# Optimization experiments

Measured on AMD Instinct MI355X. Metric: run time of the kernel, lower is better.

## Reference

```python
import jax, jax.numpy as jnp
import numpy as np

N = 50000          # nodes
E = 800000         # edges (avg degree 16)
IN_C = 3
HEADS = 4
NUM_GRAPHS = 8
NUM_CLASSES = 10


def setup_inputs() -> dict:
    key = jax.random.key(0)
    ks = jax.random.split(key, 12)
    x = jax.random.normal(ks[0], (N, IN_C), jnp.float32)
    edge_index = jax.random.randint(ks[1], (2, E), 0, N, dtype=jnp.int64)
    batch = jnp.sort(jax.random.randint(ks[2], (N,), 0, NUM_GRAPHS, dtype=jnp.int64))

    def glorot(k, shape, fan):
        return jax.random.normal(k, shape, jnp.float32) * np.float32(1.0 / np.sqrt(fan))

    return {
        "x": x, "edge_index": edge_index, "batch": batch,
        "fc0_w": glorot(ks[3], (IN_C, 16), IN_C), "fc0_b": jnp.zeros((16,), jnp.float32),
        "u1": glorot(ks[4], (16, HEADS), 16), "c1": jnp.zeros((HEADS,), jnp.float32),
        "w1": glorot(ks[5], (16, HEADS * 32), 16), "b1": jnp.zeros((32,), jnp.float32),
        "u2": glorot(ks[6], (32, HEADS), 32), "c2": jnp.zeros((HEADS,), jnp.float32),
        "w2": glorot(ks[7], (32, HEADS * 64), 32), "b2": jnp.zeros((64,), jnp.float32),
        "fc1_w": glorot(ks[8], (64, NUM_CLASSES), 64), "fc1_b": jnp.zeros((NUM_CLASSES,), jnp.float32),
    }


def feast_conv(x, src, dst, u, c, w, b, heads, out_c):
    """FeaStConv (t_inv=True): per-edge head softmax on (x_j - x_i), mean aggregation."""
    n = x.shape[0]
    # soft-assignment over heads: [E, H]
    q = jax.nn.softmax((x[src] - x[dst]) @ u + c, axis=-1)
    # transform at node level, then gather per edge: [E, H, out_c]
    xw = (x @ w).reshape(n, heads, out_c)
    msg = jnp.einsum('eh,ehc->ec', q, xw[src])           # [E, out_c]
    agg = jax.ops.segment_sum(msg, dst, num_segments=n)  # sum over incoming edges
    cnt = jax.ops.segment_sum(jnp.ones((src.shape[0],), x.dtype), dst, num_segments=n)
    return agg / jnp.maximum(cnt, 1.0)[:, None] + b


def global_mean_pool(x, batch, num_graphs):
    s = jax.ops.segment_sum(x, batch, num_segments=num_graphs)
    cnt = jax.ops.segment_sum(jnp.ones((x.shape[0],), x.dtype), batch, num_segments=num_graphs)
    return s / jnp.maximum(cnt, 1.0)[:, None]


def reference(x, edge_index, batch, fc0_w, fc0_b, u1, c1, w1, b1, u2, c2, w2, b2, fc1_w, fc1_b):
    src, dst = edge_index[0], edge_index[1]   # x_j = x[src], x_i = x[dst]
    h = jax.nn.relu(x @ fc0_w + fc0_b)                              # [N, 16]
    h = jax.nn.relu(feast_conv(h, src, dst, u1, c1, w1, b1, HEADS, 32))  # [N, 32]
    h = jax.nn.relu(feast_conv(h, src, dst, u2, c2, w2, b2, HEADS, 64))  # [N, 64]
    g = global_mean_pool(h, batch, NUM_GRAPHS)                      # [G, 64]
    # dropout is identity in eval mode
    return g @ fc1_w + fc1_b                                        # [G, num_classes]
```

## Files before the change

kernel.cpp:

```cpp
#include <hip/hip_runtime.h>

#define N_NODES 50000
#define N_EDGES 800000
#define HEADS 4
#define NUM_GRAPHS 8

#define EBLK ((N_EDGES + 255) / 256)
#define NBLK ((N_NODES + 255) / 256)

__global__ __launch_bounds__(256) void hist_fc0_kernel(
    const int* __restrict__ dst, int* __restrict__ deg, int* __restrict__ off,
    const float* __restrict__ x,
    const float* __restrict__ fc0_w, const float* __restrict__ fc0_b,
    const float* __restrict__ u1,
    float* __restrict__ h0, float* __restrict__ P1) {
  if (blockIdx.x < EBLK) {
    int e = blockIdx.x * 256 + threadIdx.x;
    if (e < N_EDGES) off[e] = atomicAdd(&deg[dst[e]], 1);
    return;
  }
  __shared__ float sW0[3 * 16];
  __shared__ float sB0[16];
  __shared__ float sU[16 * 4];
  for (int i = threadIdx.x; i < 48; i += 256) sW0[i] = fc0_w[i];
  for (int i = threadIdx.x; i < 16; i += 256) sB0[i] = fc0_b[i];
  for (int i = threadIdx.x; i < 64; i += 256) sU[i] = u1[i];
  __syncthreads();
  int n = (blockIdx.x - EBLK) * 256 + threadIdx.x;
  if (n >= N_NODES) return;
  float x0 = x[n * 3 + 0], x1 = x[n * 3 + 1], x2 = x[n * 3 + 2];
  float h[16];
#pragma unroll
  for (int j = 0; j < 16; j++) {
    float v = x0 * sW0[0 * 16 + j] + x1 * sW0[1 * 16 + j] + x2 * sW0[2 * 16 + j] + sB0[j];
    h[j] = fmaxf(v, 0.f);
    h0[(size_t)n * 16 + j] = h[j];
  }
  float p0 = 0.f, p1 = 0.f, p2 = 0.f, p3 = 0.f;
#pragma unroll
  for (int j = 0; j < 16; j++) {
    p0 += h[j] * sU[j * 4 + 0];
    p1 += h[j] * sU[j * 4 + 1];
    p2 += h[j] * sU[j * 4 + 2];
    p3 += h[j] * sU[j * 4 + 3];
  }
  reinterpret_cast<float4*>(P1)[n] = make_float4(p0, p1, p2, p3);
}

__global__ __launch_bounds__(256) void alloc_kernel(const int* __restrict__ deg,
                                                    int* __restrict__ gctr,
                                                    int* __restrict__ rowstart) {
  int i = blockIdx.x * blockDim.x + threadIdx.x;
  int lane = threadIdx.x & 63;
  int d = (i < N_NODES) ? deg[i] : 0;
  int pre = d;
#pragma unroll
  for (int offd = 1; offd < 64; offd <<= 1) {
    int v = __shfl_up(pre, offd, 64);
    if (lane >= offd) pre += v;
  }
  int total = __shfl(pre, 63, 64);
  int base = 0;
  if (lane == 63) base = atomicAdd(gctr, total);
  base = __shfl(base, 63, 64);
  if (i < N_NODES) rowstart[i] = base + pre - d;
}

__global__ __launch_bounds__(256) void scatter_kernel(const int* __restrict__ src,
                                                      const int* __restrict__ dst,
                                                      const int* __restrict__ rowstart,
                                                      const int* __restrict__ off,
                                                      int* __restrict__ src_perm) {
  int e = blockIdx.x * blockDim.x + threadIdx.x;
  if (e >= N_EDGES) return;
  src_perm[rowstart[dst[e]] + off[e]] = src[e];
}

__device__ __forceinline__ float4 edge_q(float4 Ps, float b0, float b1, float b2, float b3) {
  float l0 = Ps.x + b0, l1 = Ps.y + b1, l2 = Ps.z + b2, l3 = Ps.w + b3;
  float m = fmaxf(fmaxf(l0, l1), fmaxf(l2, l3));
  float e0 = __expf(l0 - m), e1 = __expf(l1 - m), e2 = __expf(l2 - m), e3 = __expf(l3 - m);
  float inv = 1.f / (e0 + e1 + e2 + e3);
  return make_float4(e0 * inv, e1 * inv, e2 * inv, e3 * inv);
}

__global__ __launch_bounds__(256) void agg1_kernel(
    const int* __restrict__ rowstart, const int* __restrict__ deg,
    const int* __restrict__ src_perm,
    const float* __restrict__ P1, const float* __restrict__ c1,
    const float* __restrict__ h0,
    float* __restrict__ A) {
  int wave = threadIdx.x >> 6;
  int lane = threadIdx.x & 63;
  int g = lane >> 4;
  int j = lane & 15;
  int node = blockIdx.x * 4 + wave;
  if (node >= N_NODES) return;
  float4 Pd = reinterpret_cast<const float4*>(P1)[node];
  float b0 = c1[0] - Pd.x, b1 = c1[1] - Pd.y, b2 = c1[2] - Pd.z, b3 = c1[3] - Pd.w;
  int e0 = rowstart[node];
  int e1 = e0 + deg[node];
  const float4* P4 = reinterpret_cast<const float4*>(P1);
  float a0 = 0.f, a1 = 0.f, a2 = 0.f, a3 = 0.f;
  int p = e0;
  for (; p + 16 <= e1; p += 16) {
    int sA = src_perm[p + 0 + g];
    int sB = src_perm[p + 4 + g];
    int sC = src_perm[p + 8 + g];
    int sD = src_perm[p + 12 + g];
    float4 PA = P4[sA];
    float4 PB = P4[sB];
    float4 PC = P4[sC];
    float4 PD = P4[sD];
    float fA = h0[(size_t)sA * 16 + j];
    float fB = h0[(size_t)sB * 16 + j];
    float fC = h0[(size_t)sC * 16 + j];
    float fD = h0[(size_t)sD * 16 + j];
    float4 qA = edge_q(PA, b0, b1, b2, b3);
    float4 qB = edge_q(PB, b0, b1, b2, b3);
    float4 qC = edge_q(PC, b0, b1, b2, b3);
    float4 qD = edge_q(PD, b0, b1, b2, b3);
    a0 += qA.x * fA + qB.x * fB + qC.x * fC + qD.x * fD;
    a1 += qA.y * fA + qB.y * fB + qC.y * fC + qD.y * fD;
    a2 += qA.z * fA + qB.z * fB + qC.z * fC + qD.z * fD;
    a3 += qA.w * fA + qB.w * fB + qC.w * fC + qD.w * fD;
  }
  for (; p + 4 <= e1; p += 4) {
    int s = src_perm[p + g];
    float4 Ps = P4[s];
    float f = h0[(size_t)s * 16 + j];
    float4 q = edge_q(Ps, b0, b1, b2, b3);
    a0 += q.x * f; a1 += q.y * f; a2 += q.z * f; a3 += q.w * f;
  }
  int rem = e1 - p;
  if (g < rem) {
    int s = src_perm[p + g];
    float4 Ps = P4[s];
    float f = h0[(size_t)s * 16 + j];
    float4 q = edge_q(Ps, b0, b1, b2, b3);
    a0 += q.x * f; a1 += q.y * f; a2 += q.z * f; a3 += q.w * f;
  }
  a0 += __shfl_xor(a0, 16, 64); a0 += __shfl_xor(a0, 32, 64);
  a1 += __shfl_xor(a1, 16, 64); a1 += __shfl_xor(a1, 32, 64);
  a2 += __shfl_xor(a2, 16, 64); a2 += __shfl_xor(a2, 32, 64);
  a3 += __shfl_xor(a3, 16, 64); a3 += __shfl_xor(a3, 32, 64);
  float o = (g == 0) ? a0 : (g == 1) ? a1 : (g == 2) ? a2 : a3;
  A[(size_t)node * 64 + lane] = o;
}

__global__ __launch_bounds__(256) void agg2_kernel(
    const int* __restrict__ rowstart, const int* __restrict__ deg,
    const int* __restrict__ src_perm,
    const float* __restrict__ P2, const float* __restrict__ c2,
    const float* __restrict__ h1,
    float* __restrict__ A) {
  int wave = threadIdx.x >> 6;
  int lane = threadIdx.x & 63;
  int g = lane >> 5;
  int j = lane & 31;
  int node = blockIdx.x * 4 + wave;
  if (node >= N_NODES) return;
  float4 Pd = reinterpret_cast<const float4*>(P2)[node];
  float b0 = c2[0] - Pd.x, b1 = c2[1] - Pd.y, b2 = c2[2] - Pd.z, b3 = c2[3] - Pd.w;
  int e0 = rowstart[node];
  int e1 = e0 + deg[node];
  const float4* P4 = reinterpret_cast<const float4*>(P2);
  float a0 = 0.f, a1 = 0.f, a2 = 0.f, a3 = 0.f;
  int p = e0;
  for (; p + 8 <= e1; p += 8) {
    int sA = src_perm[p + 0 + g];
    int sB = src_perm[p + 2 + g];
    int sC = src_perm[p + 4 + g];
    int sD = src_perm[p + 6 + g];
    float4 PA = P4[sA];
    float4 PB = P4[sB];
    float4 PC = P4[sC];
    float4 PD = P4[sD];
    float fA = h1[(size_t)sA * 32 + j];
    float fB = h1[(size_t)sB * 32 + j];
    float fC = h1[(size_t)sC * 32 + j];
    float fD = h1[(size_t)sD * 32 + j];
    float4 qA = edge_q(PA, b0, b1, b2, b3);
    float4 qB = edge_q(PB, b0, b1, b2, b3);
    float4 qC = edge_q(PC, b0, b1, b2, b3);
    float4 qD = edge_q(PD, b0, b1, b2, b3);
    a0 += qA.x * fA + qB.x * fB + qC.x * fC + qD.x * fD;
    a1 += qA.y * fA + qB.y * fB + qC.y * fC + qD.y * fD;
    a2 += qA.z * fA + qB.z * fB + qC.z * fC + qD.z * fD;
    a3 += qA.w * fA + qB.w * fB + qC.w * fC + qD.w * fD;
  }
  for (; p + 2 <= e1; p += 2) {
    int s = src_perm[p + g];
    float4 Ps = P4[s];
    float f = h1[(size_t)s * 32 + j];
    float4 q = edge_q(Ps, b0, b1, b2, b3);
    a0 += q.x * f; a1 += q.y * f; a2 += q.z * f; a3 += q.w * f;
  }
  int rem = e1 - p;
  if (g < rem) {
    int s = src_perm[p + g];
    float4 Ps = P4[s];
    float f = h1[(size_t)s * 32 + j];
    float4 q = edge_q(Ps, b0, b1, b2, b3);
    a0 += q.x * f; a1 += q.y * f; a2 += q.z * f; a3 += q.w * f;
  }
  a0 += __shfl_xor(a0, 32, 64);
  a1 += __shfl_xor(a1, 32, 64);
  a2 += __shfl_xor(a2, 32, 64);
  a3 += __shfl_xor(a3, 32, 64);
  float oa = (g == 0) ? a0 : a1;
  float ob = (g == 0) ? a2 : a3;
  A[(size_t)node * 128 + lane] = oa;
  A[(size_t)node * 128 + 64 + lane] = ob;
}

__global__ __launch_bounds__(256) void gemm1_kernel(
    const int* __restrict__ deg, const float* __restrict__ A,
    const float* __restrict__ w1, const float* __restrict__ b1,
    const float* __restrict__ u2,
    float* __restrict__ h1, float* __restrict__ P2) {
  __shared__ float sB[64 * 32];
  __shared__ float sU[32 * 4];
  for (int i = threadIdx.x; i < 64 * 32; i += 256) {
    int hj = i / 32, c = i % 32;
    sB[i] = w1[(hj % 16) * 128 + (hj / 16) * 32 + c];
  }
  for (int i = threadIdx.x; i < 128; i += 256) sU[i] = u2[i];
  __syncthreads();
  const float4* sB4 = reinterpret_cast<const float4*>(sB);
  int c4 = threadIdx.x & 7;
  int g = threadIdx.x >> 3;
  int n0 = blockIdx.x * 64 + g * 2;
  int n1 = n0 + 1;
  int na = min(n0, N_NODES - 1);
  int nb = min(n1, N_NODES - 1);
  const float4* A0 = reinterpret_cast<const float4*>(A + (size_t)na * 64);
  const float4* A1 = reinterpret_cast<const float4*>(A + (size_t)nb * 64);
  float4 bc = reinterpret_cast<const float4*>(b1)[c4];
  float4 acc0 = {0, 0, 0, 0}, acc1 = {0, 0, 0, 0};
#pragma unroll 2
  for (int k4 = 0; k4 < 16; k4++) {
    float4 a0 = A0[k4];
    float4 a1 = A1[k4];
    float4 w0 = sB4[(4 * k4 + 0) * 8 + c4];
    float4 wv1 = sB4[(4 * k4 + 1) * 8 + c4];
    float4 w2v = sB4[(4 * k4 + 2) * 8 + c4];
    float4 w3 = sB4[(4 * k4 + 3) * 8 + c4];
    acc0.x += a0.x * w0.x + a0.y * wv1.x + a0.z * w2v.x + a0.w * w3.x;
    acc0.y += a0.x * w0.y + a0.y * wv1.y + a0.z * w2v.y + a0.w * w3.y;
    acc0.z += a0.x * w0.z + a0.y * wv1.z + a0.z * w2v.z + a0.w * w3.z;
    acc0.w += a0.x * w0.w + a0.y * wv1.w + a0.z * w2v.w + a0.w * w3.w;
    acc1.x += a1.x * w0.x + a1.y * wv1.x + a1.z * w2v.x + a1.w * w3.x;
    acc1.y += a1.x * w0.y + a1.y * wv1.y + a1.z * w2v.y + a1.w * w3.y;
    acc1.z += a1.x * w0.z + a1.y * wv1.z + a1.z * w2v.z + a1.w * w3.z;
    acc1.w += a1.x * w0.w + a1.y * wv1.w + a1.z * w2v.w + a1.w * w3.w;
  }
  float inv0 = 1.f / fmaxf((float)deg[na], 1.f);
  float inv1 = 1.f / fmaxf((float)deg[nb], 1.f);
  float4 o0 = {fmaxf(acc0.x * inv0 + bc.x, 0.f), fmaxf(acc0.y * inv0 + bc.y, 0.f),
               fmaxf(acc0.z * inv0 + bc.z, 0.f), fmaxf(acc0.w * inv0 + bc.w, 0.f)};
  float4 o1 = {fmaxf(acc1.x * inv1 + bc.x, 0.f), fmaxf(acc1.y * inv1 + bc.y, 0.f),
               fmaxf(acc1.z * inv1 + bc.z, 0.f), fmaxf(acc1.w * inv1 + bc.w, 0.f)};
  if (n0 < N_NODES) reinterpret_cast<float4*>(h1 + (size_t)n0 * 32)[c4] = o0;
  if (n1 < N_NODES) reinterpret_cast<float4*>(h1 + (size_t)n1 * 32)[c4] = o1;
  float pa[4] = {0, 0, 0, 0}, pb[4] = {0, 0, 0, 0};
#pragma unroll
  for (int k = 0; k < 4; k++) {
    int c = 4 * c4 + k;
    float v0 = k == 0 ? o0.x : k == 1 ? o0.y : k == 2 ? o0.z : o0.w;
    float v1 = k == 0 ? o1.x : k == 1 ? o1.y : k == 2 ? o1.z : o1.w;
#pragma unroll
    for (int hh = 0; hh < 4; hh++) {
      pa[hh] += v0 * sU[c * 4 + hh];
      pb[hh] += v1 * sU[c * 4 + hh];
    }
  }
#pragma unroll
  for (int msk = 1; msk <= 4; msk <<= 1) {
#pragma unroll
    for (int hh = 0; hh < 4; hh++) {
      pa[hh] += __shfl_xor(pa[hh], msk, 64);
      pb[hh] += __shfl_xor(pb[hh], msk, 64);
    }
  }
  if (c4 == 0) {
    if (n0 < N_NODES)
      reinterpret_cast<float4*>(P2)[n0] = make_float4(pa[0], pa[1], pa[2], pa[3]);
    if (n1 < N_NODES)
      reinterpret_cast<float4*>(P2)[n1] = make_float4(pb[0], pb[1], pb[2], pb[3]);
  }
}

__global__ __launch_bounds__(256) void gemm2_kernel(
    const int* __restrict__ deg, const float* __restrict__ A,
    const float* __restrict__ w2, const float* __restrict__ b2,
    float* __restrict__ h2) {
  __shared__ float sB[128 * 64];
  for (int i = threadIdx.x; i < 128 * 64; i += 256) {
    int hj = i / 64, c = i % 64;
    sB[i] = w2[(hj % 32) * 256 + (hj / 32) * 64 + c];
  }
  __syncthreads();
  const float4* sB4 = reinterpret_cast<const float4*>(sB);
  int c4 = threadIdx.x & 15;
  int g = threadIdx.x >> 4;
  int n0 = blockIdx.x * 32 + g * 2;
  int n1 = n0 + 1;
  int na = min(n0, N_NODES - 1);
  int nb = min(n1, N_NODES - 1);
  const float4* A0 = reinterpret_cast<const float4*>(A + (size_t)na * 128);
  const float4* A1 = reinterpret_cast<const float4*>(A + (size_t)nb * 128);
  float4 bc = reinterpret_cast<const float4*>(b2)[c4];
  float4 acc0 = {0, 0, 0, 0}, acc1 = {0, 0, 0, 0};
#pragma unroll 2
  for (int k4 = 0; k4 < 32; k4++) {
    float4 a0 = A0[k4];
    float4 a1 = A1[k4];
    float4 w0 = sB4[(4 * k4 + 0) * 16 + c4];
    float4 wv1 = sB4[(4 * k4 + 1) * 16 + c4];
    float4 w2v = sB4[(4 * k4 + 2) * 16 + c4];
    float4 w3 = sB4[(4 * k4 + 3) * 16 + c4];
    acc0.x += a0.x * w0.x + a0.y * wv1.x + a0.z * w2v.x + a0.w * w3.x;
    acc0.y += a0.x * w0.y + a0.y * wv1.y + a0.z * w2v.y + a0.w * w3.y;
    acc0.z += a0.x * w0.z + a0.y * wv1.z + a0.z * w2v.z + a0.w * w3.z;
    acc0.w += a0.x * w0.w + a0.y * wv1.w + a0.z * w2v.w + a0.w * w3.w;
    acc1.x += a1.x * w0.x + a1.y * wv1.x + a1.z * w2v.x + a1.w * w3.x;
    acc1.y += a1.x * w0.y + a1.y * wv1.y + a1.z * w2v.y + a1.w * w3.y;
    acc1.z += a1.x * w0.z + a1.y * wv1.z + a1.z * w2v.z + a1.w * w3.z;
    acc1.w += a1.x * w0.w + a1.y * wv1.w + a1.z * w2v.w + a1.w * w3.w;
  }
  if (n0 < N_NODES) {
    float inv = 1.f / fmaxf((float)deg[n0], 1.f);
    float4 o = {fmaxf(acc0.x * inv + bc.x, 0.f), fmaxf(acc0.y * inv + bc.y, 0.f),
                fmaxf(acc0.z * inv + bc.z, 0.f), fmaxf(acc0.w * inv + bc.w, 0.f)};
    reinterpret_cast<float4*>(h2 + (size_t)n0 * 64)[c4] = o;
  }
  if (n1 < N_NODES) {
    float inv = 1.f / fmaxf((float)deg[n1], 1.f);
    float4 o = {fmaxf(acc1.x * inv + bc.x, 0.f), fmaxf(acc1.y * inv + bc.y, 0.f),
                fmaxf(acc1.z * inv + bc.z, 0.f), fmaxf(acc1.w * inv + bc.w, 0.f)};
    reinterpret_cast<float4*>(h2 + (size_t)n1 * 64)[c4] = o;
  }
}

#define POOL_CHUNK 64
__global__ __launch_bounds__(256) void pool_kernel(
    const float* __restrict__ h2, const int* __restrict__ batch,
    float* __restrict__ gsum, float* __restrict__ gcnt) {
  int grp = threadIdx.x / 64;
  int c = threadIdx.x % 64;
  int n0 = (blockIdx.x * 4 + grp) * POOL_CHUNK;
  int n1 = min(n0 + POOL_CHUNK, N_NODES);
  if (n0 >= N_NODES) return;
  float acc = 0.f;
  float cacc = 0.f;
  int curg = batch[n0];
  for (int n = n0; n < n1; n++) {
    int g = batch[n];
    float v = h2[(size_t)n * 64 + c];
    if (g != curg) {
      atomicAdd(&gsum[curg * 64 + c], acc);
      if (c == 0) atomicAdd(&gcnt[curg], cacc);
      acc = 0.f;
      cacc = 0.f;
      curg = g;
    }
    acc += v;
    cacc += 1.f;
  }
  atomicAdd(&gsum[curg * 64 + c], acc);
  if (c == 0) atomicAdd(&gcnt[curg], cacc);
}

__global__ __launch_bounds__(128) void head_kernel(
    const float* __restrict__ gsum, const float* __restrict__ gcnt,
    const float* __restrict__ fc1_w, const float* __restrict__ fc1_b,
    float* __restrict__ out) {
  int t = threadIdx.x;
  if (t >= NUM_GRAPHS * 10) return;
  int g = t / 10, k = t % 10;
  float inv = 1.f / fmaxf(gcnt[g], 1.f);
  float s = fc1_b[k];
#pragma unroll
  for (int c = 0; c < 64; c++) s += gsum[g * 64 + c] * inv * fc1_w[c * 10 + k];
  out[g * 10 + k] = s;
}

extern "C" void kernel_launch(void* const* d_in, const int* in_sizes, int n_in,
                              void* d_out, int out_size, void* d_ws, size_t ws_size,
                              hipStream_t stream) {
  const float* x = (const float*)d_in[0];
  const int* edge_index = (const int*)d_in[1];
  const int* batch = (const int*)d_in[2];
  const float* fc0_w = (const float*)d_in[3];
  const float* fc0_b = (const float*)d_in[4];
  const float* u1 = (const float*)d_in[5];
  const float* c1 = (const float*)d_in[6];
  const float* w1 = (const float*)d_in[7];
  const float* b1 = (const float*)d_in[8];
  const float* u2 = (const float*)d_in[9];
  const float* c2 = (const float*)d_in[10];
  const float* w2 = (const float*)d_in[11];
  const float* b2 = (const float*)d_in[12];
  const float* fc1_w = (const float*)d_in[13];
  const float* fc1_b = (const float*)d_in[14];
  float* out = (float*)d_out;

  const int* src = edge_index;
  const int* dst = edge_index + N_EDGES;

  char* wsb = (char*)d_ws;
  int* deg = (int*)wsb;
  int* gctr = deg + N_NODES;
  float* gsum = (float*)wsb + 50004;
  float* gcnt = gsum + NUM_GRAPHS * 64;
  int* rowstart = (int*)wsb + 50524;
  int* off = rowstart + N_NODES;
  int* src_perm = off + N_EDGES;
  float* h0 = (float*)wsb + 1700524;
  float* h1 = h0 + (size_t)N_NODES * 16;
  float* h2 = h1 + (size_t)N_NODES * 32;
  float* A = h2 + (size_t)N_NODES * 64;
  float* P1 = A + (size_t)N_NODES * 128;
  float* P2 = P1 + (size_t)N_NODES * 4;

  hipMemsetAsync(d_ws, 0, 50524 * sizeof(int), stream);

  int nblk = NBLK;
  int eblk = EBLK;
  int wblk = (N_NODES + 3) / 4;

  hist_fc0_kernel<<<eblk + nblk, 256, 0, stream>>>(dst, deg, off, x, fc0_w, fc0_b, u1, h0, P1);
  alloc_kernel<<<nblk, 256, 0, stream>>>(deg, gctr, rowstart);
  scatter_kernel<<<eblk, 256, 0, stream>>>(src, dst, rowstart, off, src_perm);

  agg1_kernel<<<wblk, 256, 0, stream>>>(rowstart, deg, src_perm, P1, c1, h0, A);
  gemm1_kernel<<<(N_NODES + 63) / 64, 256, 0, stream>>>(deg, A, w1, b1, u2, h1, P2);

  agg2_kernel<<<wblk, 256, 0, stream>>>(rowstart, deg, src_perm, P2, c2, h1, A);
  gemm2_kernel<<<(N_NODES + 31) / 32, 256, 0, stream>>>(deg, A, w2, b2, h2);

  int pblk = (N_NODES + POOL_CHUNK * 4 - 1) / (POOL_CHUNK * 4);
  pool_kernel<<<pblk, 256, 0, stream>>>(h2, batch, gsum, gcnt);
  head_kernel<<<1, 128, 0, stream>>>(gsum, gcnt, fc1_w, fc1_b, out);
}
```

Baseline: 273.3 us.

## Fuse gemm2 with global mean pooling and classifier head via last-block pattern

The layer-2 GEMM epilogue now accumulates each node's output directly into per-block shared-memory graph sums, then flushes them with global atomics. This removes the h2 write and reread and the separate pool kernel. The last block to finish, detected with an atomic counter, computes the final classifier output, which removes the head kernel launch. In exchange it adds shared and global atomics plus a threadfence and counter handshake, and relies on batch being sorted so that most blocks span at most two graphs.

```diff
diff --git a/kernel.cpp b/kernel.cpp
--- a/kernel.cpp
+++ b/kernel.cpp
@@ -291,20 +291,35 @@
   }
 }
 
-__global__ __launch_bounds__(256) void gemm2_kernel(
+__global__ __launch_bounds__(256) void gemm2_pool_kernel(
     const int* __restrict__ deg, const float* __restrict__ A,
     const float* __restrict__ w2, const float* __restrict__ b2,
-    float* __restrict__ h2) {
+    const int* __restrict__ batch,
+    float* __restrict__ gsum, float* __restrict__ gcnt, int* __restrict__ done,
+    const float* __restrict__ fc1_w, const float* __restrict__ fc1_b,
+    float* __restrict__ out) {
   __shared__ float sB[128 * 64];
+  __shared__ float sg[2][64];
+  __shared__ float scnt[2];
+  __shared__ int sgmin, sgmax, islast;
   for (int i = threadIdx.x; i < 128 * 64; i += 256) {
     int hj = i / 64, c = i % 64;
     sB[i] = w2[(hj % 32) * 256 + (hj / 32) * 64 + c];
   }
+  if (threadIdx.x < 128) sg[threadIdx.x >> 6][threadIdx.x & 63] = 0.f;
+  if (threadIdx.x < 2) scnt[threadIdx.x] = 0.f;
+  if (threadIdx.x == 0) {
+    int base = (int)blockIdx.x * 32;
+    int last = base + 31;
+    if (last > N_NODES - 1) last = N_NODES - 1;
+    sgmin = batch[base];
+    sgmax = batch[last];
+  }
   __syncthreads();
   const float4* sB4 = reinterpret_cast<const float4*>(sB);
   int c4 = threadIdx.x & 15;
   int g = threadIdx.x >> 4;
-  int n0 = blockIdx.x * 32 + g * 2;
+  int n0 = (int)blockIdx.x * 32 + g * 2;
   int n1 = n0 + 1;
   int na = min(n0, N_NODES - 1);
   int nb = min(n1, N_NODES - 1);
@@ -329,61 +344,76 @@
     acc1.z += a1.x * w0.z + a1.y * wv1.z + a1.z * w2v.z + a1.w * w3.z;
     acc1.w += a1.x * w0.w + a1.y * wv1.w + a1.z * w2v.w + a1.w * w3.w;
   }
+  float inv0 = 1.f / fmaxf((float)deg[na], 1.f);
+  float inv1 = 1.f / fmaxf((float)deg[nb], 1.f);
+  float4 o0 = {fmaxf(acc0.x * inv0 + bc.x, 0.f), fmaxf(acc0.y * inv0 + bc.y, 0.f),
+               fmaxf(acc0.z * inv0 + bc.z, 0.f), fmaxf(acc0.w * inv0 + bc.w, 0.f)};
+  float4 o1 = {fmaxf(acc1.x * inv1 + bc.x, 0.f), fmaxf(acc1.y * inv1 + bc.y, 0.f),
+               fmaxf(acc1.z * inv1 + bc.z, 0.f), fmaxf(acc1.w * inv1 + bc.w, 0.f)};
+  int gmin = sgmin;
   if (n0 < N_NODES) {
-    float inv = 1.f / fmaxf((float)deg[n0], 1.f);
-    float4 o = {fmaxf(acc0.x * inv + bc.x, 0.f), fmaxf(acc0.y * inv + bc.y, 0.f),
-                fmaxf(acc0.z * inv + bc.z, 0.f), fmaxf(acc0.w * inv + bc.w, 0.f)};
-    reinterpret_cast<float4*>(h2 + (size_t)n0 * 64)[c4] = o;
+    int b0v = batch[na];
+    int slot = b0v - gmin;
+    if (slot <= 1) {
+      atomicAdd(&sg[slot][c4 * 4 + 0], o0.x);
+      atomicAdd(&sg[slot][c4 * 4 + 1], o0.y);
+      atomicAdd(&sg[slot][c4 * 4 + 2], o0.z);
+      atomicAdd(&sg[slot][c4 * 4 + 3], o0.w);
+      if (c4 == 0) atomicAdd(&scnt[slot], 1.f);
+    } else {
+      atomicAdd(&gsum[b0v * 64 + c4 * 4 + 0], o0.x);
+      atomicAdd(&gsum[b0v * 64 + c4 * 4 + 1], o0.y);
+      atomicAdd(&gsum[b0v * 64 + c4 * 4 + 2], o0.z);
+      atomicAdd(&gsum[b0v * 64 + c4 * 4 + 3], o0.w);
+      if (c4 == 0) atomicAdd(&gcnt[b0v], 1.f);
+    }
   }
   if (n1 < N_NODES) {
-    float inv = 1.f / fmaxf((float)deg[n1], 1.f);
-    float4 o = {fmaxf(acc1.x * inv + bc.x, 0.f), fmaxf(acc1.y * inv + bc.y, 0.f),
-                fmaxf(acc1.z * inv + bc.z, 0.f), fmaxf(acc1.w * inv + bc.w, 0.f)};
-    reinterpret_cast<float4*>(h2 + (size_t)n1 * 64)[c4] = o;
-  }
-}
-
-#define POOL_CHUNK 64
-__global__ __launch_bounds__(256) void pool_kernel(
-    const float* __restrict__ h2, const int* __restrict__ batch,
-    float* __restrict__ gsum, float* __restrict__ gcnt) {
-  int grp = threadIdx.x / 64;
-  int c = threadIdx.x % 64;
-  int n0 = (blockIdx.x * 4 + grp) * POOL_CHUNK;
-  int n1 = min(n0 + POOL_CHUNK, N_NODES);
-  if (n0 >= N_NODES) return;
-  float acc = 0.f;
-  float cacc = 0.f;
-  int curg = batch[n0];
-  for (int n = n0; n < n1; n++) {
-    int g = batch[n];
-    float v = h2[(size_t)n * 64 + c];
-    if (g != curg) {
-      atomicAdd(&gsum[curg * 64 + c], acc);
-      if (c == 0) atomicAdd(&gcnt[curg], cacc);
-      acc = 0.f;
-      cacc = 0.f;
-      curg = g;
-    }
-    acc += v;
-    cacc += 1.f;
-  }
-  atomicAdd(&gsum[curg * 64 + c], acc);
-  if (c == 0) atomicAdd(&gcnt[curg], cacc);
-}
-
-__global__ __launch_bounds__(128) void head_kernel(
-    const float* __restrict__ gsum, const float* __restrict__ gcnt,
-    const float* __restrict__ fc1_w, const float* __restrict__ fc1_b,
-    float* __restrict__ out) {
-  int t = threadIdx.x;
-  if (t >= NUM_GRAPHS * 10) return;
-  int g = t / 10, k = t % 10;
-  float inv = 1.f / fmaxf(gcnt[g], 1.f);
-  float s = fc1_b[k];
-#pragma unroll
-  for (int c = 0; c < 64; c++) s += gsum[g * 64 + c] * inv * fc1_w[c * 10 + k];
-  out[g * 10 + k] = s;
+    int b1v = batch[nb];
+    int slot = b1v - gmin;
+    if (slot <= 1) {
+      atomicAdd(&sg[slot][c4 * 4 + 0], o1.x);
+      atomicAdd(&sg[slot][c4 * 4 + 1], o1.y);
+      atomicAdd(&sg[slot][c4 * 4 + 2], o1.z);
+      atomicAdd(&sg[slot][c4 * 4 + 3], o1.w);
+      if (c4 == 0) atomicAdd(&scnt[slot], 1.f);
+    } else {
+      atomicAdd(&gsum[b1v * 64 + c4 * 4 + 0], o1.x);
+      atomicAdd(&gsum[b1v * 64 + c4 * 4 + 1], o1.y);
+      atomicAdd(&gsum[b1v * 64 + c4 * 4 + 2], o1.z);
+      atomicAdd(&gsum[b1v * 64 + c4 * 4 + 3], o1.w);
+      if (c4 == 0) atomicAdd(&gcnt[b1v], 1.f);
+    }
+  }
+  __syncthreads();
+  if (threadIdx.x < 128) {
+    int slot = threadIdx.x >> 6, ch = threadIdx.x & 63;
+    if (slot == 0 || sgmax > sgmin) {
+      int gg = sgmin + slot;
+      atomicAdd(&gsum[gg * 64 + ch], sg[slot][ch]);
+      if (ch == 0) atomicAdd(&gcnt[gg], scnt[slot]);
+    }
+  }
+  __threadfence();
+  __syncthreads();
+  if (threadIdx.x == 0) islast = (atomicAdd(done, 1) == (int)gridDim.x - 1) ? 1 : 0;
+  __syncthreads();
+  if (islast) {
+    __threadfence();
+    int t = threadIdx.x;
+    if (t < NUM_GRAPHS * 10) {
+      int gg = t / 10, k = t % 10;
+      float cntv = __hip_atomic_load(&gcnt[gg], __ATOMIC_RELAXED, __HIP_MEMORY_SCOPE_AGENT);
+      float inv = 1.f / fmaxf(cntv, 1.f);
+      float s = fc1_b[k];
+#pragma unroll
+      for (int c = 0; c < 64; c++) {
+        float sv = __hip_atomic_load(&gsum[gg * 64 + c], __ATOMIC_RELAXED, __HIP_MEMORY_SCOPE_AGENT);
+        s += sv * inv * fc1_w[c * 10 + k];
+      }
+      out[gg * 10 + k] = s;
+    }
+  }
 }
 
 extern "C" void kernel_launch(void* const* d_in, const int* in_sizes, int n_in,
@@ -412,6 +442,7 @@
   char* wsb = (char*)d_ws;
   int* deg = (int*)wsb;
   int* gctr = deg + N_NODES;
+  int* done = gctr + 1;
   float* gsum = (float*)wsb + 50004;
   float* gcnt = gsum + NUM_GRAPHS * 64;
   int* rowstart = (int*)wsb + 50524;
@@ -419,12 +450,11 @@
   int* src_perm = off + N_EDGES;
   float* h0 = (float*)wsb + 1700524;
   float* h1 = h0 + (size_t)N_NODES * 16;
-  float* h2 = h1 + (size_t)N_NODES * 32;
-  float* A = h2 + (size_t)N_NODES * 64;
+  float* A = h1 + (size_t)N_NODES * 32;
   float* P1 = A + (size_t)N_NODES * 128;
   float* P2 = P1 + (size_t)N_NODES * 4;
 
-  hipMemsetAsync(d_ws, 0, 50524 * sizeof(int), stream);
+  (void)hipMemsetAsync(d_ws, 0, 50524 * sizeof(int), stream);
 
   int nblk = NBLK;
   int eblk = EBLK;
@@ -438,9 +468,6 @@
   gemm1_kernel<<<(N_NODES + 63) / 64, 256, 0, stream>>>(deg, A, w1, b1, u2, h1, P2);
 
   agg2_kernel<<<wblk, 256, 0, stream>>>(rowstart, deg, src_perm, P2, c2, h1, A);
-  gemm2_kernel<<<(N_NODES + 31) / 32, 256, 0, stream>>>(deg, A, w2, b2, h2);
-
-  int pblk = (N_NODES + POOL_CHUNK * 4 - 1) / (POOL_CHUNK * 4);
-  pool_kernel<<<pblk, 256, 0, stream>>>(h2, batch, gsum, gcnt);
-  head_kernel<<<1, 128, 0, stream>>>(gsum, gcnt, fc1_w, fc1_b, out);
-}
+  gemm2_pool_kernel<<<(N_NODES + 31) / 32, 256, 0, stream>>>(
+      deg, A, w2, b2, batch, gsum, gcnt, done, fc1_w, fc1_b, out);
+}
```

New measurement: 344.2 us. +26.0%, slower.
